# Optimization experiments

Measured on AMD Instinct MI355X. Metric: run time of the kernel, lower is better.

Reference implementation:

```python
import jax, jax.numpy as jnp
import numpy as np

B, H, W, Q, E, M, K, WIN = 4, 192, 192, 160, 96, 96, 4, 7
NO_ELECTRON_WEIGHT = 0.1


def _bce_logits(x, z):
    # binary_cross_entropy_with_logits, elementwise: softplus(x) - x*z
    return jnp.logaddexp(0.0, x) - x * z


def setup_inputs() -> dict:
    key = jax.random.key(0)
    ks = jax.random.split(key, 11)
    is_electron_logit = jax.random.normal(ks[0], (B * Q,), jnp.float32)
    true_segmap = jax.random.uniform(ks[1], (B, H, W, E), jnp.float32)
    binary_mask_logits = jax.random.normal(ks[2], (B, H, W, Q), jnp.float32)
    portion_logits = jax.random.normal(ks[3], (B, H, W, Q), jnp.float32)
    # keep incidence points away from borders so the 7x7 window stays in-bounds
    incidence_points = jax.random.uniform(ks[4], (B, E, 2), jnp.float32) * (H - 8) + 4.0
    positions = jax.random.uniform(ks[5], (B, Q, 2), jnp.float32) * H
    a = jax.random.normal(ks[6], (B, Q, 3), jnp.float32)
    l00 = jax.nn.softplus(a[..., 0]) + 0.1
    l11 = jax.nn.softplus(a[..., 2]) + 0.1
    l10 = 0.5 * a[..., 1]
    zero = jnp.zeros_like(l00)
    chol = jnp.stack([jnp.stack([l00, zero], -1), jnp.stack([l10, l11], -1)], -2)  # [B,Q,2,2] lower-tri
    occupancy_logits = jax.random.normal(ks[7], (B, H, W, K), jnp.float32)
    occupancy_true = jax.random.randint(ks[8], (B, H, W), 0, K, jnp.int32)
    qkeys = jax.random.split(ks[9], B)
    matched_q = jnp.stack([jax.random.permutation(k, Q)[:M] for k in qkeys]).astype(jnp.int32)
    ekeys = jax.random.split(ks[10], B)
    matched_e = jnp.stack([jax.random.permutation(k, E) for k in ekeys]).astype(jnp.int32)
    return dict(is_electron_logit=is_electron_logit, true_segmap=true_segmap,
                binary_mask_logits=binary_mask_logits, portion_logits=portion_logits,
                incidence_points=incidence_points, positions=positions, chol=chol,
                occupancy_logits=occupancy_logits, occupancy_true=occupancy_true,
                matched_q=matched_q, matched_e=matched_e)


def reference(is_electron_logit, true_segmap, binary_mask_logits, portion_logits,
              incidence_points, positions, chol, occupancy_logits, occupancy_true,
              matched_q, matched_e):
    # ---- class loss (weighted BCE over flat per-query logits) ----
    labels = jnp.zeros((B * Q,), is_electron_logit.dtype)
    glob = (jnp.arange(B)[:, None] * Q + matched_q).reshape(-1)
    labels = labels.at[glob].set(1.0)
    weights = jnp.where(labels > 0, 1.0, NO_ELECTRON_WEIGHT).astype(is_electron_logit.dtype)
    class_loss = jnp.mean(weights * _bce_logits(is_electron_logit, labels))

    # ---- reorder segmentation maps to matched order (_reorder_segmentation_map) ----
    true_r = jnp.take_along_axis(true_segmap, matched_e[:, None, None, :], axis=3)        # [B,H,W,M]
    bin_r = jnp.take_along_axis(binary_mask_logits, matched_q[:, None, None, :], axis=3)  # [B,H,W,M]
    por_r = jnp.take_along_axis(portion_logits, matched_q[:, None, None, :], axis=3)      # [B,H,W,M]

    # ---- mask BCE on 7x7 windows around floor(matched incidence point) ----
    pts_r = jnp.take_along_axis(incidence_points, matched_e[..., None], axis=1)  # [B,M,2]
    pix = jnp.floor(pts_r).astype(jnp.int32)
    half = WIN // 2
    dr = jnp.arange(-half, half + 1)
    rows = pix[..., 0][:, :, None, None] + dr[None, None, :, None]  # [B,M,7,1]
    cols = pix[..., 1][:, :, None, None] + dr[None, None, None, :]  # [B,M,1,7]
    bi = jnp.arange(B)[:, None, None, None]
    mi = jnp.arange(M)[None, :, None, None]
    tv = true_r[bi, rows, cols, mi]  # [B,M,7,7]
    lg = bin_r[bi, rows, cols, mi]
    bce_loss = jnp.mean(_bce_logits(lg, tv))

    # ---- dice loss (softmax over matched-electron dim) ----
    portion = jax.nn.softmax(por_r, axis=-1)
    num = jnp.sum(2.0 * true_r * portion, axis=(1, 2, 3))
    den = jnp.sum(true_r + portion, axis=(1, 2, 3))
    dice_loss = jnp.mean(1.0 - (num + 1.0) / (den + 1.0))

    # ---- distance NLL (2D MVN with lower-tri scale) ----
    centers_r = jnp.take_along_axis(positions, matched_q[..., None], axis=1)       # [B,M,2]
    chol_r = jnp.take_along_axis(chol, matched_q[..., None, None], axis=1)         # [B,M,2,2]
    d = pts_r - centers_r
    z0 = d[..., 0] / chol_r[..., 0, 0]
    z1 = (d[..., 1] - chol_r[..., 1, 0] * z0) / chol_r[..., 1, 1]
    nll = 0.5 * (z0 * z0 + z1 * z1) + jnp.log(2.0 * jnp.pi) \
          + jnp.log(chol_r[..., 0, 0]) + jnp.log(chol_r[..., 1, 1])
    nll = jnp.where(jnp.isinf(nll), 1e7, nll)
    nll_loss = jnp.mean(nll)

    # ---- occupancy loss (per-pixel electron-count cross-entropy) ----
    logp = jax.nn.log_softmax(occupancy_logits, axis=-1)
    occ_loss = -jnp.mean(jnp.take_along_axis(logp, occupancy_true[..., None], axis=-1))

    # loss_weights all 1.0 (defaults); dot(weights, terms)
    return class_loss + bce_loss + dice_loss + nll_loss + occ_loss
```

## Files before the change

### kernel.cpp

```cpp
#include <hip/hip_runtime.h>
#include <math.h>

#define B_ 4
#define H_ 192
#define W_ 192
#define Q_ 160
#define E_ 96
#define M_ 96
#define HW_ (H_ * W_)
#define NPIX_ (B_ * HW_)
#define NTILE 9
#define WTILE_B 4096
#define NDICE 1024
#define NSMALL 962
#define NBUCKET 64
#define WS_NUM0 4
#define WS_TS0  260
#define WS_TOTAL 516

__device__ __forceinline__ void stage16(const void* g, void* l) {
    __builtin_amdgcn_global_load_lds(
        (const __attribute__((address_space(1))) void*)g,
        (__attribute__((address_space(3))) void*)l, 16, 0, 0);
}

template <int CTRL, int RMASK>
__device__ __forceinline__ float dpp_add_step(float x) {
    int v = __builtin_amdgcn_update_dpp(0, __float_as_int(x), CTRL, RMASK, 0xF, false);
    return x + __int_as_float(v);
}
__device__ __forceinline__ float wave_sum63(float x) {
    x = dpp_add_step<0x111, 0xF>(x);
    x = dpp_add_step<0x112, 0xF>(x);
    x = dpp_add_step<0x114, 0xF>(x);
    x = dpp_add_step<0x118, 0xF>(x);
    x = dpp_add_step<0x142, 0xA>(x);
    x = dpp_add_step<0x143, 0xC>(x);
    return x;
}

__device__ __forceinline__ float waveSumAll(float v) {
    for (int m = 32; m > 0; m >>= 1) v += __shfl_xor(v, m, 64);
    return v;
}

__device__ __forceinline__ float softplusf(float x) {
    return fmaxf(x, 0.f) + log1pf(__expf(-fabsf(x)));
}

__global__ __launch_bounds__(256) void fused_kernel(
    const float* __restrict__ logit,
    const float* __restrict__ trueseg,
    const float* __restrict__ binlog,
    const float* __restrict__ por,
    const float* __restrict__ inc,
    const float* __restrict__ pos,
    const float* __restrict__ chol,
    const float* __restrict__ occlog,
    const int* __restrict__ occtrue,
    const int* __restrict__ mqall,
    const int* __restrict__ meall,
    float* __restrict__ ws)
{
    __shared__ float tilebuf[4 * 2 * WTILE_B / 4];
    const int tid  = threadIdx.x;
    const int lane = tid & 63;
    const int wid  = tid >> 6;
    const int blk  = blockIdx.x;

    if (blk < NDICE) {
        const int b = blk >> 8;
        const int slot = blk & 255;
        const bool hi = lane < 32;
        const int l31 = lane & 31;
        const int* mq = mqall + b * M_;
        const int* me = meall + b * M_;
        const int mqa = mq[lane];
        const int mea = me[lane];
        const int mqb = mq[64 + l31];
        const int meb = me[64 + l31];
        const float m1 = hi ? 1.f : 0.f;

        const char* porb = (const char*)(por + (size_t)b * HW_ * Q_);
        const char* trb  = (const char*)(trueseg + (size_t)b * HW_ * E_);

        asm volatile("s_waitcnt vmcnt(0)" ::: "memory");

        char* wbase = (char*)tilebuf + wid * (2 * WTILE_B);

        float an = 0.f;
        float at = 0.f;

        #define STAGE(t_) do {                                                 \
            const int p0_ = (slot + (t_) * 256) * 16 + wid * 4;                \
            const char* gp_ = porb + (size_t)p0_ * 640;                        \
            const char* gt_ = trb  + (size_t)p0_ * 384;                        \
            char* dst_ = wbase + ((t_) & 1) * WTILE_B;                         \
            _Pragma("unroll")                                                  \
            for (int i_ = 0; i_ < 4; ++i_) {                                   \
                const int off_ = i_ * 1024 + lane * 16;                        \
                const char* s_ = (off_ < 2560) ? (gp_ + off_)                  \
                                               : (gt_ + (off_ - 2560));        \
                stage16(s_, dst_ + i_ * 1024);                                 \
            }                                                                  \
        } while (0)

        #define COMP(t_) do {                                                  \
            const float* pl_ = (const float*)(wbase + ((t_) & 1) * WTILE_B);   \
            const float* tl_ = pl_ + 640;                                      \
            _Pragma("unroll")                                                  \
            for (int k_ = 0; k_ < 4; ++k_) {                                   \
                float p0v_ = pl_[k_ * Q_ + mqa];                               \
                float t0_  = tl_[k_ * E_ + mea];                               \
                float p1_  = pl_[k_ * Q_ + mqb];                               \
                float t1_  = tl_[k_ * E_ + meb];                               \
                float e0_ = __expf(p0v_);                                      \
                float e1_ = __expf(p1_) * m1;                                  \
                float s_  = wave_sum63(e0_ + e1_);                             \
                float se_ = wave_sum63(fmaf(t1_, e1_, t0_ * e0_));             \
                an += __fdividef(se_, s_);                                     \
                at += fmaf(t1_, m1, t0_);                                      \
            }                                                                  \
        } while (0)

        STAGE(0); STAGE(1);

        for (int t = 0; t < NTILE - 2; ++t) {
            asm volatile("s_waitcnt vmcnt(4)" ::: "memory");
            COMP(t);
            asm volatile("s_waitcnt lgkmcnt(0)" ::: "memory");
            STAGE(t + 2);
        }
        asm volatile("s_waitcnt vmcnt(4)" ::: "memory");
        COMP(NTILE - 2);
        asm volatile("s_waitcnt vmcnt(0)" ::: "memory");
        COMP(NTILE - 1);

        #undef STAGE
        #undef COMP

        float atr = wave_sum63(at);
        if (lane == 63) {
            int bucket = blk & (NBUCKET - 1);
            atomicAdd(&ws[WS_NUM0 + bucket * 4 + b], 2.f * an);
            atomicAdd(&ws[WS_TS0  + bucket * 4 + b], atr);
        }
    } else {
        float* lab = tilebuf;
        const int s = blk - NDICE;
        float acc = 0.f;
        if (s == 0) {
            for (int i = tid; i < B_ * Q_; i += 256) lab[i] = 0.f;
            __syncthreads();
            for (int i = tid; i < B_ * M_; i += 256) {
                int b = i / M_;
                lab[b * Q_ + mqall[i]] = 1.f;
            }
            __syncthreads();
            for (int i = tid; i < B_ * Q_; i += 256) {
                float x = logit[i];
                float z = lab[i];
                float w = z > 0.f ? 1.f : 0.1f;
                acc += w * (softplusf(x) - x * z);
            }
            float wsum = wave_sum63(acc);
            if (lane == 63) atomicAdd(&ws[0], wsum);
        } else if (s == 1) {
            for (int i = tid; i < B_ * M_; i += 256) {
                int b = i / M_;
                int qi = mqall[i];
                int ei = meall[i];
                float px = inc[(b * E_ + ei) * 2 + 0];
                float py = inc[(b * E_ + ei) * 2 + 1];
                float cx = pos[(b * Q_ + qi) * 2 + 0];
                float cy = pos[(b * Q_ + qi) * 2 + 1];
                const float* ch = chol + (size_t)(b * Q_ + qi) * 4;
                float l00 = ch[0], l10 = ch[2], l11 = ch[3];
                float d0 = px - cx, d1 = py - cy;
                float z0 = d0 / l00;
                float z1 = (d1 - l10 * z0) / l11;
                float nll = 0.5f * (z0 * z0 + z1 * z1) + 1.837877066409345f
                            + logf(l00) + logf(l11);
                if (isinf(nll)) nll = 1e7f;
                acc += nll;
            }
            float wsum = wave_sum63(acc);
            if (lane == 63) atomicAdd(&ws[2], wsum);
        } else if (s < 386) {
            int idx = s - 2;
            int b = idx / M_;
            int ei = meall[idx];
            int qi = mqall[idx];
            float px = inc[(b * E_ + ei) * 2 + 0];
            float py = inc[(b * E_ + ei) * 2 + 1];
            int r0 = (int)floorf(px) - 3;
            int c0 = (int)floorf(py) - 3;
            if (tid < 49) {
                int rr = r0 + tid / 7;
                int cc = c0 + tid % 7;
                size_t pix = ((size_t)b * H_ + rr) * W_ + cc;
                float tv = trueseg[pix * E_ + ei];
                float lg = binlog[pix * Q_ + qi];
                acc = softplusf(lg) - lg * tv;
            }
            if (wid == 0) {
                float wsum = wave_sum63(acc);
                if (lane == 63) atomicAdd(&ws[1], wsum);
            }
        } else {
            int p = (s - 386) * 256 + tid;
            if (p < NPIX_) {
                float4 v = *(const float4*)(occlog + (size_t)p * 4);
                int lb = occtrue[p];
                float m = fmaxf(fmaxf(v.x, v.y), fmaxf(v.z, v.w));
                float lse = m + __logf(__expf(v.x - m) + __expf(v.y - m) +
                                       __expf(v.z - m) + __expf(v.w - m));
                float xs = lb == 0 ? v.x : (lb == 1 ? v.y : (lb == 2 ? v.z : v.w));
                acc = lse - xs;
            }
            float wsum = wave_sum63(acc);
            if (lane == 63) atomicAdd(&ws[3], wsum);
        }
    }
}

__global__ __launch_bounds__(64) void final_kernel(const float* __restrict__ ws,
                                                   float* __restrict__ out)
{
    const int lane = threadIdx.x;
    float n[B_], t[B_];
    for (int b = 0; b < B_; ++b) {
        n[b] = waveSumAll(ws[WS_NUM0 + lane * 4 + b]);
        t[b] = waveSumAll(ws[WS_TS0  + lane * 4 + b]);
    }
    if (lane == 0) {
        float class_l = ws[0] * (1.f / (B_ * Q_));
        float bce_l   = ws[1] * (1.f / (B_ * M_ * 49));
        float nll_l   = ws[2] * (1.f / (B_ * M_));
        float occ_l   = ws[3] * (1.f / NPIX_);
        float dice = 0.f;
        for (int b = 0; b < B_; ++b)
            dice += 1.f - (n[b] + 1.f) / (t[b] + (float)HW_ + 1.f);
        dice *= (1.f / B_);
        out[0] = class_l + bce_l + nll_l + occ_l + dice;
    }
}

extern "C" void kernel_launch(void* const* d_in, const int* in_sizes, int n_in,
                              void* d_out, int out_size, void* d_ws, size_t ws_size,
                              hipStream_t stream) {
    const float* logit   = (const float*)d_in[0];
    const float* trueseg = (const float*)d_in[1];
    const float* binlog  = (const float*)d_in[2];
    const float* por     = (const float*)d_in[3];
    const float* inc     = (const float*)d_in[4];
    const float* pos     = (const float*)d_in[5];
    const float* chol    = (const float*)d_in[6];
    const float* occlog  = (const float*)d_in[7];
    const int*   occtrue = (const int*)d_in[8];
    const int*   mq      = (const int*)d_in[9];
    const int*   me      = (const int*)d_in[10];
    float* out = (float*)d_out;
    float* ws  = (float*)d_ws;

    (void)hipMemsetAsync(d_ws, 0, WS_TOTAL * sizeof(float), stream);

    hipLaunchKernelGGL(fused_kernel, dim3(NDICE + NSMALL), dim3(256), 0, stream,
                       logit, trueseg, binlog, por, inc, pos, chol, occlog, occtrue,
                       mq, me, ws);
    hipLaunchKernelGGL(final_kernel, dim3(1), dim3(64), 0, stream, ws, out);
}
```

Before: 262.9 us.

## Read trueseg directly via inverse permutation and share portion tiles block-wide

Builds the inverse of matched_e in LDS so each lane loads trueseg in natural electron order straight into registers, with coalesced loads. The portion index is gathered through mq[inv_me[e]] instead. Portion tiles are now staged into one block-shared double buffer, and __syncthreads replaces the hand-placed per-wave vmcnt waits. This is meant to shrink LDS traffic and the scattered trueseg gathers. In exchange it adds block-wide barriers that drain outstanding loads, so the pipeline runs only one tile ahead.

```diff
diff --git a/kernel.cpp b/kernel.cpp
--- a/kernel.cpp
+++ b/kernel.cpp
@@ -9,8 +9,9 @@
 #define M_ 96
 #define HW_ (H_ * W_)
 #define NPIX_ (B_ * HW_)
+#define TPIX 16
 #define NTILE 9
-#define WTILE_B 4096
+#define PORT_B (TPIX * Q_ * 4)
 #define NDICE 1024
 #define NSMALL 962
 #define NBUCKET 64
@@ -62,7 +63,9 @@
     const int* __restrict__ meall,
     float* __restrict__ ws)
 {
-    __shared__ float tilebuf[4 * 2 * WTILE_B / 4];
+    __shared__ float tilebuf[2 * TPIX * Q_];
+    __shared__ int   smq[M_];
+    __shared__ int   sinv[M_];
     const int tid  = threadIdx.x;
     const int lane = tid & 63;
     const int wid  = tid >> 6;
@@ -75,68 +78,72 @@
         const int l31 = lane & 31;
         const int* mq = mqall + b * M_;
         const int* me = meall + b * M_;
-        const int mqa = mq[lane];
-        const int mea = me[lane];
-        const int mqb = mq[64 + l31];
-        const int meb = me[64 + l31];
+        if (tid < M_) { smq[tid] = mq[tid]; sinv[me[tid]] = tid; }
+        __syncthreads();
+        const int pqa = smq[sinv[lane]];
+        const int pqb = smq[sinv[64 + l31]];
         const float m1 = hi ? 1.f : 0.f;
 
         const char* porb = (const char*)(por + (size_t)b * HW_ * Q_);
         const char* trb  = (const char*)(trueseg + (size_t)b * HW_ * E_);
 
-        asm volatile("s_waitcnt vmcnt(0)" ::: "memory");
-
-        char* wbase = (char*)tilebuf + wid * (2 * WTILE_B);
-
         float an = 0.f;
         float at = 0.f;
+        float tcur[8], tnxt[8];
 
         #define STAGE(t_) do {                                                 \
-            const int p0_ = (slot + (t_) * 256) * 16 + wid * 4;                \
+            const int p0_ = (slot + (t_) * 256) * TPIX;                        \
             const char* gp_ = porb + (size_t)p0_ * 640;                        \
-            const char* gt_ = trb  + (size_t)p0_ * 384;                        \
-            char* dst_ = wbase + ((t_) & 1) * WTILE_B;                         \
+            char* db_ = (char*)tilebuf + ((t_) & 1) * PORT_B;                  \
+            for (int i_ = wid; i_ < 10; i_ += 4)                               \
+                stage16(gp_ + i_ * 1024 + lane * 16, db_ + i_ * 1024);         \
+        } while (0)
+
+        #define TLOAD(t_, dst_) do {                                           \
+            const int p0_ = (slot + (t_) * 256) * TPIX + wid * 4;              \
+            const char* gt_ = trb + (size_t)p0_ * 384;                         \
             _Pragma("unroll")                                                  \
-            for (int i_ = 0; i_ < 4; ++i_) {                                   \
-                const int off_ = i_ * 1024 + lane * 16;                        \
-                const char* s_ = (off_ < 2560) ? (gp_ + off_)                  \
-                                               : (gt_ + (off_ - 2560));        \
-                stage16(s_, dst_ + i_ * 1024);                                 \
+            for (int k_ = 0; k_ < 4; ++k_) {                                   \
+                dst_[k_]     = *(const float*)(gt_ + k_ * 384 + lane * 4);     \
+                dst_[4 + k_] = *(const float*)(gt_ + k_ * 384 + 256 + l31 * 4);\
             }                                                                  \
         } while (0)
 
-        #define COMP(t_) do {                                                  \
-            const float* pl_ = (const float*)(wbase + ((t_) & 1) * WTILE_B);   \
-            const float* tl_ = pl_ + 640;                                      \
+        #define COMP(t_, tc_) do {                                             \
+            const float* pl_ = tilebuf + ((t_) & 1) * (TPIX * Q_);             \
             _Pragma("unroll")                                                  \
             for (int k_ = 0; k_ < 4; ++k_) {                                   \
-                float p0v_ = pl_[k_ * Q_ + mqa];                               \
-                float t0_  = tl_[k_ * E_ + mea];                               \
-                float p1_  = pl_[k_ * Q_ + mqb];                               \
-                float t1_  = tl_[k_ * E_ + meb];                               \
-                float e0_ = __expf(p0v_);                                      \
-                float e1_ = __expf(p1_) * m1;                                  \
+                const int pix_ = wid * 4 + k_;                                 \
+                float e0_ = __expf(pl_[pix_ * Q_ + pqa]);                      \
+                float e1_ = __expf(pl_[pix_ * Q_ + pqb]) * m1;                 \
+                float t0_ = tc_[k_];                                           \
+                float t1_ = tc_[4 + k_] * m1;                                  \
                 float s_  = wave_sum63(e0_ + e1_);                             \
                 float se_ = wave_sum63(fmaf(t1_, e1_, t0_ * e0_));             \
                 an += __fdividef(se_, s_);                                     \
-                at += fmaf(t1_, m1, t0_);                                      \
+                at += t0_ + t1_;                                               \
             }                                                                  \
         } while (0)
 
-        STAGE(0); STAGE(1);
-
-        for (int t = 0; t < NTILE - 2; ++t) {
-            asm volatile("s_waitcnt vmcnt(4)" ::: "memory");
-            COMP(t);
-            asm volatile("s_waitcnt lgkmcnt(0)" ::: "memory");
+        STAGE(0);
+        TLOAD(0, tcur);
+
+        for (int tt = 0; tt < 4; ++tt) {
+            const int t = 2 * tt;
+            __syncthreads();
+            STAGE(t + 1);
+            TLOAD(t + 1, tnxt);
+            COMP(t, tcur);
+            __syncthreads();
             STAGE(t + 2);
+            TLOAD(t + 2, tcur);
+            COMP(t + 1, tnxt);
         }
-        asm volatile("s_waitcnt vmcnt(4)" ::: "memory");
-        COMP(NTILE - 2);
-        asm volatile("s_waitcnt vmcnt(0)" ::: "memory");
-        COMP(NTILE - 1);
+        __syncthreads();
+        COMP(8, tcur);
 
         #undef STAGE
+        #undef TLOAD
         #undef COMP
 
         float atr = wave_sum63(at);
```

New measurement: 255.6 us. 1.03x faster.
